# Kernel optimization log

Hardware: AMD Instinct MI355X
Metric: run time of the kernel (lower is better)

Reference implementation:

```python
import jax, jax.numpy as jnp
import numpy as np

B, S, D = 4, 4096, 1024
E, H, TOPK = 8, 2752, 2


def setup_inputs() -> dict:
    key = jax.random.key(0)
    k0, k1, k2, k3, k4 = jax.random.split(key, 5)
    x = jax.random.normal(k0, (B, S, D), dtype=jnp.float32)
    gate_w = jax.random.normal(k1, (E, D), dtype=jnp.float32) * 0.02
    w1 = jax.random.normal(k2, (E, H, D), dtype=jnp.float32) * 0.02
    w2 = jax.random.normal(k3, (E, D, H), dtype=jnp.float32) * 0.02
    w3 = jax.random.normal(k4, (E, H, D), dtype=jnp.float32) * 0.02
    return {"x": x, "gate_w": gate_w, "w1": w1, "w2": w2, "w3": w3}


def reference(x, gate_w, w1, w2, w3):
    """MoE layer: softmax router -> top-k (normalized) -> per-expert SwiGLU FFN -> weighted combine."""
    b, s, d = x.shape
    xt = x.reshape(-1, d)                       # [T, D], T = B*S
    logits = xt @ gate_w.T                      # [T, E]
    scores = jax.nn.softmax(logits, axis=-1)
    topk_w, topk_i = jax.lax.top_k(scores, TOPK)  # [T, K]
    topk_w = topk_w / (jnp.sum(topk_w, axis=-1, keepdims=True) + 1e-20)

    y = jnp.zeros_like(xt)
    n_experts = gate_w.shape[0]
    for e in range(n_experts):
        # combine weight for expert e per token (0 if not routed to e)
        we = jnp.sum(jnp.where(topk_i == e, topk_w, 0.0), axis=-1)  # [T]
        h = jax.nn.silu(xt @ w1[e].T) * (xt @ w3[e].T)              # [T, H]
        y = y + we[:, None] * (h @ w2[e].T)                         # [T, D]
    return y.reshape(b, s, d)
```

## Files before the change

kernel.cpp:

```cpp
#include <hip/hip_runtime.h>
#include <hip/hip_bf16.h>
#include <stdint.h>

#define T_TOK 16384
#define D_DIM 1024
#define E_NUM 8
#define H_DIM 2752
#define NSLOT (T_TOK * 2)

typedef __bf16 bf16x8_t __attribute__((ext_vector_type(8)));
typedef float f32x4_t __attribute__((ext_vector_type(4)));

__device__ __forceinline__ uint16_t f2bf(float f) {
    union { float f; uint32_t u; } v; v.f = f;
    return (uint16_t)((v.u + 0x7FFFu + ((v.u >> 16) & 1u)) >> 16);
}
__device__ __forceinline__ ushort4 f4_to_bf4(float4 v) {
    ushort4 r; r.x = f2bf(v.x); r.y = f2bf(v.y); r.z = f2bf(v.z); r.w = f2bf(v.w);
    return r;
}
__device__ __forceinline__ void gl_lds16(const uint16_t* g, uint16_t* l) {
    __builtin_amdgcn_global_load_lds((const __attribute__((address_space(1))) void*)g,
                                     (__attribute__((address_space(3))) void*)l,
                                     16, 0, 0);
}

__global__ __launch_bounds__(256) void router_kernel(
    const float* __restrict__ x, const float* __restrict__ gw,
    int* __restrict__ topk_i, float* __restrict__ topk_w) {
    int tid = threadIdx.x;
    int t = blockIdx.x * 4 + (tid >> 6);
    int lane = tid & 63;
    const float* xr = x + (size_t)t * D_DIM;
    double acc[E_NUM];
#pragma unroll
    for (int e = 0; e < E_NUM; ++e) acc[e] = 0.0;
    for (int k = lane; k < D_DIM; k += 64) {
        double xv = (double)xr[k];
#pragma unroll
        for (int e = 0; e < E_NUM; ++e) acc[e] += xv * (double)gw[e * D_DIM + k];
    }
#pragma unroll
    for (int e = 0; e < E_NUM; ++e) {
        double v = acc[e];
        for (int off = 32; off > 0; off >>= 1) v += __shfl_down(v, off, 64);
        acc[e] = v;
    }
    if (lane == 0) {
        int i0 = 0; double m0 = acc[0];
#pragma unroll
        for (int e = 1; e < E_NUM; ++e) if (acc[e] > m0) { m0 = acc[e]; i0 = e; }
        int i1 = -1; double m1 = -1.0e300;
#pragma unroll
        for (int e = 0; e < E_NUM; ++e) if (e != i0 && acc[e] > m1) { m1 = acc[e]; i1 = e; }
        double e1 = exp(m1 - m0);
        double s = 1.0 + e1;
        topk_i[t * 2 + 0] = i0; topk_i[t * 2 + 1] = i1;
        topk_w[t * 2 + 0] = (float)(1.0 / s);
        topk_w[t * 2 + 1] = (float)(e1 / s);
    }
}

__global__ __launch_bounds__(256) void count_kernel(
    const int* __restrict__ topk_i,
    int* __restrict__ counts_f, int* __restrict__ counts_s) {
    __shared__ int hf[E_NUM], hs[E_NUM];
    int tid = threadIdx.x;
    if (tid < E_NUM) { hf[tid] = 0; hs[tid] = 0; }
    __syncthreads();
    int t = blockIdx.x * 256 + tid;
    atomicAdd(&hf[topk_i[t * 2 + 0]], 1);
    atomicAdd(&hs[topk_i[t * 2 + 1]], 1);
    __syncthreads();
    if (tid < E_NUM) {
        if (hf[tid]) atomicAdd(&counts_f[tid], hf[tid]);
    } else if (tid < 2 * E_NUM) {
        int e = tid - E_NUM;
        if (hs[e]) atomicAdd(&counts_s[e], hs[e]);
    }
}

__global__ void prefix_kernel(const int* __restrict__ cf, const int* __restrict__ cs,
                              int* __restrict__ bases, int* __restrict__ splits,
                              int* __restrict__ cnts) {
    int s = 0;
    for (int e = 0; e < E_NUM; ++e) {
        bases[e] = s;
        splits[e] = s + cf[e];
        cnts[e] = cf[e] + cs[e];
        s += cnts[e];
    }
}

__global__ __launch_bounds__(256) void assign_kernel(
    const int* __restrict__ topk_i, const float* __restrict__ topk_w,
    const int* __restrict__ bases, const int* __restrict__ splits,
    int* __restrict__ fills_f, int* __restrict__ fills_s,
    int* __restrict__ slot_tok, float* __restrict__ slot_w) {
    __shared__ int hf[E_NUM], hs[E_NUM], bf[E_NUM], bs[E_NUM];
    int tid = threadIdx.x;
    if (tid < E_NUM) { hf[tid] = 0; hs[tid] = 0; }
    __syncthreads();
    int t = blockIdx.x * 256 + tid;
    int e0 = topk_i[t * 2 + 0], e1 = topk_i[t * 2 + 1];
    int r0 = atomicAdd(&hf[e0], 1);
    int r1 = atomicAdd(&hs[e1], 1);
    __syncthreads();
    if (tid < E_NUM) {
        bf[tid] = hf[tid] ? atomicAdd(&fills_f[tid], hf[tid]) : 0;
    } else if (tid < 2 * E_NUM) {
        int e = tid - E_NUM;
        bs[e] = hs[e] ? atomicAdd(&fills_s[e], hs[e]) : 0;
    }
    __syncthreads();
    int s0 = bases[e0] + bf[e0] + r0;
    int s1 = splits[e1] + bs[e1] + r1;
    slot_tok[s0] = t; slot_w[s0] = topk_w[t * 2 + 0];
    slot_tok[s1] = t; slot_w[s1] = topk_w[t * 2 + 1];
}

__global__ __launch_bounds__(256) void cvtx_kernel(const float* __restrict__ x,
                                                   uint16_t* __restrict__ Xb) {
    size_t i = (size_t)blockIdx.x * 256 + threadIdx.x;
    ((ushort4*)Xb)[i] = f4_to_bf4(((const float4*)x)[i]);
}
__global__ __launch_bounds__(256) void cvt13g_kernel(const float* __restrict__ w1,
                                                     const float* __restrict__ w3,
                                                     uint16_t* __restrict__ w1be,
                                                     uint16_t* __restrict__ w3be, int g) {
    size_t i = (size_t)blockIdx.x * 256 + threadIdx.x;
    size_t off = (size_t)g * 4 * H_DIM * D_DIM / 4;
    ((ushort4*)w1be)[i] = f4_to_bf4(((const float4*)w1)[off + i]);
    ((ushort4*)w3be)[i] = f4_to_bf4(((const float4*)w3)[off + i]);
}
__global__ __launch_bounds__(256) void cvt2_kernel(const float* __restrict__ w2,
                                                   uint16_t* __restrict__ w2b) {
    size_t i = (size_t)blockIdx.x * 256 + threadIdx.x;
    ((ushort4*)w2b)[i] = f4_to_bf4(((const float4*)w2)[i]);
}


__global__ __launch_bounds__(256) void gemm1_kernel(
    const uint16_t* __restrict__ Xb, const uint16_t* __restrict__ w1be,
    const uint16_t* __restrict__ w3be, const int* __restrict__ slot_tok,
    const int* __restrict__ cnts, const int* __restrict__ bases,
    uint16_t* __restrict__ hidden, int g) {
    int ez = blockIdx.z;
    int e = g * 4 + ez;
    int cnt = cnts[e];
    int m0 = blockIdx.y * 128;
    if (m0 >= cnt) return;
    int n0 = blockIdx.x * 64;
    int base = bases[e];
    const uint16_t* w1p = w1be + (size_t)ez * H_DIM * D_DIM;
    const uint16_t* w3p = w3be + (size_t)ez * H_DIM * D_DIM;

    __shared__ __align__(16) uint16_t As[3][128 * 32];
    __shared__ __align__(16) uint16_t B1s[3][64 * 32];
    __shared__ __align__(16) uint16_t B3s[3][64 * 32];

    int tid = threadIdx.x;
    int w = tid >> 6, lane = tid & 63;
    int rA = lane & 15, kq = lane >> 4;
    int lr = lane >> 2, lc = lane & 3;
    int slr = (lr >> 1) & 3;
    int ks = kq ^ ((rA >> 1) & 3);

    int tok0 = slot_tok[base + min(m0 + w * 32 + lr, cnt - 1)];
    int tok1 = slot_tok[base + min(m0 + w * 32 + 16 + lr, cnt - 1)];
    const uint16_t* pA0 = Xb + (size_t)tok0 * D_DIM + (lc ^ slr) * 8;
    const uint16_t* pA1 = Xb + (size_t)tok1 * D_DIM + (lc ^ slr) * 8;
    const uint16_t* pB1 = w1p + (size_t)(n0 + w * 16 + lr) * D_DIM + (lc ^ slr) * 8;
    const uint16_t* pB3 = w3p + (size_t)(n0 + w * 16 + lr) * D_DIM + (lc ^ slr) * 8;

    f32x4_t acc1[2][4], acc3[2][4];
#pragma unroll
    for (int r = 0; r < 2; ++r)
#pragma unroll
        for (int n = 0; n < 4; ++n) {
            acc1[r][n] = (f32x4_t){0.f, 0.f, 0.f, 0.f};
            acc3[r][n] = (f32x4_t){0.f, 0.f, 0.f, 0.f};
        }

#define G1_STAGE(bi) do {                                   \
        gl_lds16(pA0, &As[bi][(w * 2 + 0) * 512]);          \
        gl_lds16(pA1, &As[bi][(w * 2 + 1) * 512]);          \
        gl_lds16(pB1, &B1s[bi][w * 512]);                   \
        gl_lds16(pB3, &B3s[bi][w * 512]);                   \
        pA0 += 32; pA1 += 32; pB1 += 32; pB3 += 32; } while (0)

    G1_STAGE(0);
    G1_STAGE(1);
    for (int t = 0; t < 32; ++t) {
        if (t < 31) { asm volatile("s_waitcnt vmcnt(4)" ::: "memory"); }
        else        { asm volatile("s_waitcnt vmcnt(0)" ::: "memory"); }
        __builtin_amdgcn_s_barrier();
        if (t < 30) G1_STAGE((t + 2) % 3);
        int c = t % 3;

        bf16x8_t a0 = *(const bf16x8_t*)&As[c][(w * 32 + rA) * 32 + ks * 8];
        bf16x8_t a1 = *(const bf16x8_t*)&As[c][(w * 32 + 16 + rA) * 32 + ks * 8];
#pragma unroll
        for (int n = 0; n < 4; ++n) {
            bf16x8_t b1 = *(const bf16x8_t*)&B1s[c][(n * 16 + rA) * 32 + ks * 8];
            bf16x8_t b3 = *(const bf16x8_t*)&B3s[c][(n * 16 + rA) * 32 + ks * 8];
            acc1[0][n] = __builtin_amdgcn_mfma_f32_16x16x32_bf16(a0, b1, acc1[0][n], 0, 0, 0);
            acc1[1][n] = __builtin_amdgcn_mfma_f32_16x16x32_bf16(a1, b1, acc1[1][n], 0, 0, 0);
            acc3[0][n] = __builtin_amdgcn_mfma_f32_16x16x32_bf16(a0, b3, acc3[0][n], 0, 0, 0);
            acc3[1][n] = __builtin_amdgcn_mfma_f32_16x16x32_bf16(a1, b3, acc3[1][n], 0, 0, 0);
        }
    }
#undef G1_STAGE

#pragma unroll
    for (int r = 0; r < 2; ++r)
#pragma unroll
        for (int n = 0; n < 4; ++n)
#pragma unroll
            for (int i = 0; i < 4; ++i) {
                int mrow = m0 + w * 32 + r * 16 + kq * 4 + i;
                if (mrow < cnt) {
                    float gv = acc1[r][n][i];
                    float s = gv / (1.0f + __expf(-gv));
                    float h = s * acc3[r][n][i];
                    hidden[(size_t)(base + mrow) * H_DIM + n0 + n * 16 + rA] = f2bf(h);
                }
            }
}

__global__ __launch_bounds__(256) void gemm2_kernel(
    const uint16_t* __restrict__ hidden, const uint16_t* __restrict__ w2b,
    const int* __restrict__ cnts, const int* __restrict__ bases,
    const int* __restrict__ slot_tok, const float* __restrict__ slot_w,
    float* __restrict__ out) {
    int e = blockIdx.z;
    int cnt = cnts[e];
    int lin = blockIdx.y * 8 + blockIdx.x;
    int c8 = lin & 7, j = lin >> 3;
    int m_t = (j >> 3) * 8 + c8;
    int x_t = j & 7;
    int m0 = m_t * 128;
    if (m0 >= cnt) return;
    int base = bases[e];
    int d0 = x_t * 128;

    __shared__ __align__(16) uint16_t As[3][128 * 32];
    __shared__ __align__(16) uint16_t Bs[3][128 * 32];

    int tid = threadIdx.x;
    int w = tid >> 6, lane = tid & 63;
    int rA = lane & 15, kq = lane >> 4;
    int lr = lane >> 2, lc = lane & 3;
    int slr = (lr >> 1) & 3;
    int ks = kq ^ ((rA >> 1) & 3);
    int mh = w & 1, nh = w >> 1;

    int sl0 = base + min(m0 + w * 32 + lr, cnt - 1);
    int sl1 = base + min(m0 + w * 32 + 16 + lr, cnt - 1);
    const uint16_t* pA0 = hidden + (size_t)sl0 * H_DIM + (lc ^ slr) * 8;
    const uint16_t* pA1 = hidden + (size_t)sl1 * H_DIM + (lc ^ slr) * 8;
    const uint16_t* pB0 = w2b + (size_t)(e * D_DIM + d0 + w * 32 + lr) * H_DIM + (lc ^ slr) * 8;
    const uint16_t* pB1 = w2b + (size_t)(e * D_DIM + d0 + w * 32 + 16 + lr) * H_DIM + (lc ^ slr) * 8;

    f32x4_t acc[4][4];
#pragma unroll
    for (int mf = 0; mf < 4; ++mf)
#pragma unroll
        for (int nf = 0; nf < 4; ++nf) acc[mf][nf] = (f32x4_t){0.f, 0.f, 0.f, 0.f};

#define G2_STAGE(bi) do {                                   \
        gl_lds16(pA0, &As[bi][(w * 2 + 0) * 512]);          \
        gl_lds16(pA1, &As[bi][(w * 2 + 1) * 512]);          \
        gl_lds16(pB0, &Bs[bi][(w * 2 + 0) * 512]);          \
        gl_lds16(pB1, &Bs[bi][(w * 2 + 1) * 512]);          \
        pA0 += 32; pA1 += 32; pB0 += 32; pB1 += 32; } while (0)

    G2_STAGE(0);
    G2_STAGE(1);
    for (int t = 0; t < 86; ++t) {
        if (t < 85) { asm volatile("s_waitcnt vmcnt(4)" ::: "memory"); }
        else        { asm volatile("s_waitcnt vmcnt(0)" ::: "memory"); }
        __builtin_amdgcn_s_barrier();
        if (t < 84) G2_STAGE((t + 2) % 3);
        int c = t % 3;

        bf16x8_t a[4], b[4];
#pragma unroll
        for (int mf = 0; mf < 4; ++mf)
            a[mf] = *(const bf16x8_t*)&As[c][(mh * 64 + mf * 16 + rA) * 32 + ks * 8];
#pragma unroll
        for (int nf = 0; nf < 4; ++nf)
            b[nf] = *(const bf16x8_t*)&Bs[c][(nh * 64 + nf * 16 + rA) * 32 + ks * 8];
#pragma unroll
        for (int mf = 0; mf < 4; ++mf)
#pragma unroll
            for (int nf = 0; nf < 4; ++nf)
                acc[mf][nf] = __builtin_amdgcn_mfma_f32_16x16x32_bf16(a[mf], b[nf], acc[mf][nf], 0, 0, 0);
    }
#undef G2_STAGE

#pragma unroll
    for (int mf = 0; mf < 4; ++mf)
#pragma unroll
        for (int i = 0; i < 4; ++i) {
            int mr = m0 + mh * 64 + mf * 16 + kq * 4 + i;
            if (mr < cnt) {
                int slot = base + mr;
                float wgt = slot_w[slot];
                int tok = slot_tok[slot];
                float* yr = out + (size_t)tok * D_DIM + d0 + nh * 64;
#pragma unroll
                for (int nf = 0; nf < 4; ++nf)
                    atomicAdd(&yr[nf * 16 + rA], wgt * acc[mf][nf][i]);
            }
        }
}

extern "C" void kernel_launch(void* const* d_in, const int* in_sizes, int n_in,
                              void* d_out, int out_size, void* d_ws, size_t ws_size,
                              hipStream_t stream) {
    const float* x  = (const float*)d_in[0];
    const float* gw = (const float*)d_in[1];
    const float* w1 = (const float*)d_in[2];
    const float* w2 = (const float*)d_in[3];
    const float* w3 = (const float*)d_in[4];
    float* out = (float*)d_out;
    char* ws = (char*)d_ws;

    int*   counts_f = (int*)(ws + 0);
    int*   counts_s = (int*)(ws + 256);
    int*   fills_f  = (int*)(ws + 512);
    int*   fills_s  = (int*)(ws + 768);
    int*   bases    = (int*)(ws + 1024);
    int*   splits   = (int*)(ws + 1280);
    int*   cnts     = (int*)(ws + 1536);
    int*   topk_i   = (int*)(ws + 4096);
    float* topk_w   = (float*)(ws + 4096 + 1 * 131072);
    int*   slot_tok = (int*)(ws + 4096 + 2 * 131072);
    float* slot_w   = (float*)(ws + 4096 + 3 * 131072);

    const size_t HID_OFF = 4ull << 20;
    const size_t W_OFF   = HID_OFF + (size_t)NSLOT * H_DIM * 2;
    const size_t W1SZ    = (size_t)H_DIM * D_DIM * 2;
    uint16_t* hidden = (uint16_t*)(ws + HID_OFF);
    uint16_t* w1be   = (uint16_t*)(ws + W_OFF);
    uint16_t* w3be   = (uint16_t*)(ws + W_OFF + 4 * W1SZ);
    uint16_t* w2b    = (uint16_t*)(ws + W_OFF);
    uint16_t* Xb     = (uint16_t*)d_out;

    hipMemsetAsync(ws, 0, 1024, stream);

    router_kernel<<<T_TOK / 4, 256, 0, stream>>>(x, gw, topk_i, topk_w);
    count_kernel<<<T_TOK / 256, 256, 0, stream>>>(topk_i, counts_f, counts_s);
    prefix_kernel<<<1, 1, 0, stream>>>(counts_f, counts_s, bases, splits, cnts);
    assign_kernel<<<T_TOK / 256, 256, 0, stream>>>(topk_i, topk_w, bases, splits,
                                                   fills_f, fills_s, slot_tok, slot_w);
    cvtx_kernel<<<T_TOK * D_DIM / 1024, 256, 0, stream>>>(x, Xb);

    for (int g = 0; g < 2; ++g) {
        cvt13g_kernel<<<H_DIM * 4, 256, 0, stream>>>(w1, w3, w1be, w3be, g);
        gemm1_kernel<<<dim3(H_DIM / 64, 128, 4), 256, 0, stream>>>(
            Xb, w1be, w3be, slot_tok, cnts, bases, hidden, g);
    }

    hipMemsetAsync(out, 0, (size_t)T_TOK * D_DIM * sizeof(float), stream);
    cvt2_kernel<<<E_NUM * D_DIM * H_DIM / 1024, 256, 0, stream>>>(w2, w2b);
    gemm2_kernel<<<dim3(8, 128, E_NUM), 256, 0, stream>>>(
        hidden, w2b, cnts, bases, slot_tok, slot_w, out);
}
```

Baseline: 1.274 ms.

## Enlarge MoE GEMM tiles to 256-row, 8-wave blocks with interleaved load/MFMA phases

Both expert GEMMs move from 256-thread blocks with 128x64 or 128x128 tiles to 512-thread blocks with 256x128 (gemm1) and 256x256 (gemm2) tiles. Each K-step is split into four phases that alternate LDS fragment reads, global-to-LDS prefetch issue and MFMA bursts, using barriers, sched_barrier and s_setprio. The aim is more data reuse per byte loaded and better overlap of memory traffic with matrix math. In exchange the kernels use more LDS and registers per block, add more barriers, and launch fewer blocks; the H dimension now needs bounds guards because 2752 is not a multiple of 128.

After: 1.291 ms. Within noise of the previous version (+1.4%).

```diff
diff --git a/kernel.cpp b/kernel.cpp
--- a/kernel.cpp
+++ b/kernel.cpp
@@ -24,6 +24,8 @@
                                      (__attribute__((address_space(3))) void*)l,
                                      16, 0, 0);
 }
+
+#define MFMA16(a, b, c) __builtin_amdgcn_mfma_f32_16x16x32_bf16(a, b, c, 0, 0, 0)
 
 __global__ __launch_bounds__(256) void router_kernel(
     const float* __restrict__ x, const float* __restrict__ gw,
@@ -140,7 +142,7 @@
 }
 
 
-__global__ __launch_bounds__(256) void gemm1_kernel(
+__global__ __launch_bounds__(512, 2) void gemm1_kernel(
     const uint16_t* __restrict__ Xb, const uint16_t* __restrict__ w1be,
     const uint16_t* __restrict__ w3be, const int* __restrict__ slot_tok,
     const int* __restrict__ cnts, const int* __restrict__ bases,
@@ -148,167 +150,285 @@
     int ez = blockIdx.z;
     int e = g * 4 + ez;
     int cnt = cnts[e];
-    int m0 = blockIdx.y * 128;
+    int m0 = blockIdx.y * 256;
     if (m0 >= cnt) return;
-    int n0 = blockIdx.x * 64;
+    int n0 = blockIdx.x * 128;
     int base = bases[e];
     const uint16_t* w1p = w1be + (size_t)ez * H_DIM * D_DIM;
     const uint16_t* w3p = w3be + (size_t)ez * H_DIM * D_DIM;
 
-    __shared__ __align__(16) uint16_t As[3][128 * 32];
-    __shared__ __align__(16) uint16_t B1s[3][64 * 32];
-    __shared__ __align__(16) uint16_t B3s[3][64 * 32];
+    __shared__ __align__(16) uint16_t As[3][256 * 32];
+    __shared__ __align__(16) uint16_t B1s[3][128 * 32];
+    __shared__ __align__(16) uint16_t B3s[3][128 * 32];
 
     int tid = threadIdx.x;
     int w = tid >> 6, lane = tid & 63;
+    int wr = w >> 2, wc = w & 3;
     int rA = lane & 15, kq = lane >> 4;
-    int lr = lane >> 2, lc = lane & 3;
-    int slr = (lr >> 1) & 3;
     int ks = kq ^ ((rA >> 1) & 3);
-
-    int tok0 = slot_tok[base + min(m0 + w * 32 + lr, cnt - 1)];
-    int tok1 = slot_tok[base + min(m0 + w * 32 + 16 + lr, cnt - 1)];
-    const uint16_t* pA0 = Xb + (size_t)tok0 * D_DIM + (lc ^ slr) * 8;
-    const uint16_t* pA1 = Xb + (size_t)tok1 * D_DIM + (lc ^ slr) * 8;
-    const uint16_t* pB1 = w1p + (size_t)(n0 + w * 16 + lr) * D_DIM + (lc ^ slr) * 8;
-    const uint16_t* pB3 = w3p + (size_t)(n0 + w * 16 + lr) * D_DIM + (lc ^ slr) * 8;
-
-    f32x4_t acc1[2][4], acc3[2][4];
-#pragma unroll
-    for (int r = 0; r < 2; ++r)
-#pragma unroll
-        for (int n = 0; n < 4; ++n) {
-            acc1[r][n] = (f32x4_t){0.f, 0.f, 0.f, 0.f};
-            acc3[r][n] = (f32x4_t){0.f, 0.f, 0.f, 0.f};
-        }
-
-#define G1_STAGE(bi) do {                                   \
-        gl_lds16(pA0, &As[bi][(w * 2 + 0) * 512]);          \
-        gl_lds16(pA1, &As[bi][(w * 2 + 1) * 512]);          \
-        gl_lds16(pB1, &B1s[bi][w * 512]);                   \
-        gl_lds16(pB3, &B3s[bi][w * 512]);                   \
-        pA0 += 32; pA1 += 32; pB1 += 32; pB3 += 32; } while (0)
-
-    G1_STAGE(0);
-    G1_STAGE(1);
+    int r = tid >> 2, c = tid & 3;
+    int cs = c ^ ((r >> 1) & 3);
+
+    int slA0 = base + min(m0 + r, cnt - 1);
+    int slA1 = base + min(m0 + 128 + r, cnt - 1);
+    const uint16_t* pA0 = Xb + (size_t)slot_tok[slA0] * D_DIM + cs * 8;
+    const uint16_t* pA1 = Xb + (size_t)slot_tok[slA1] * D_DIM + cs * 8;
+    int nB = min(n0 + r, H_DIM - 1);
+    const uint16_t* pB1 = w1p + (size_t)nB * D_DIM + cs * 8;
+    const uint16_t* pB3 = w3p + (size_t)nB * D_DIM + cs * 8;
+
+    f32x4_t acc1[8][2], acc3[8][2];
+#pragma unroll
+    for (int mf = 0; mf < 8; ++mf)
+#pragma unroll
+        for (int nf = 0; nf < 2; ++nf) {
+            acc1[mf][nf] = (f32x4_t){0.f, 0.f, 0.f, 0.f};
+            acc3[mf][nf] = (f32x4_t){0.f, 0.f, 0.f, 0.f};
+        }
+
+#define G1_STA0(s) gl_lds16(pA0, &As[s][w * 512])
+#define G1_STA1(s) gl_lds16(pA1, &As[s][4096 + w * 512])
+#define G1_STB1(s) gl_lds16(pB1, &B1s[s][w * 512])
+#define G1_STB3(s) gl_lds16(pB3, &B3s[s][w * 512])
+#define G1_ADV() do { pA0 += 32; pA1 += 32; pB1 += 32; pB3 += 32; } while (0)
+
+    G1_STA0(0); G1_STA1(0); G1_STB1(0); G1_STB3(0); G1_ADV();
+    G1_STA0(1); G1_STA1(1); G1_STB1(1); G1_STB3(1); G1_ADV();
+    asm volatile("s_waitcnt vmcnt(4)" ::: "memory");
+    __builtin_amdgcn_s_barrier();
+
     for (int t = 0; t < 32; ++t) {
-        if (t < 31) { asm volatile("s_waitcnt vmcnt(4)" ::: "memory"); }
-        else        { asm volatile("s_waitcnt vmcnt(0)" ::: "memory"); }
-        __builtin_amdgcn_s_barrier();
-        if (t < 30) G1_STAGE((t + 2) % 3);
-        int c = t % 3;
-
-        bf16x8_t a0 = *(const bf16x8_t*)&As[c][(w * 32 + rA) * 32 + ks * 8];
-        bf16x8_t a1 = *(const bf16x8_t*)&As[c][(w * 32 + 16 + rA) * 32 + ks * 8];
-#pragma unroll
-        for (int n = 0; n < 4; ++n) {
-            bf16x8_t b1 = *(const bf16x8_t*)&B1s[c][(n * 16 + rA) * 32 + ks * 8];
-            bf16x8_t b3 = *(const bf16x8_t*)&B3s[c][(n * 16 + rA) * 32 + ks * 8];
-            acc1[0][n] = __builtin_amdgcn_mfma_f32_16x16x32_bf16(a0, b1, acc1[0][n], 0, 0, 0);
-            acc1[1][n] = __builtin_amdgcn_mfma_f32_16x16x32_bf16(a1, b1, acc1[1][n], 0, 0, 0);
-            acc3[0][n] = __builtin_amdgcn_mfma_f32_16x16x32_bf16(a0, b3, acc3[0][n], 0, 0, 0);
-            acc3[1][n] = __builtin_amdgcn_mfma_f32_16x16x32_bf16(a1, b3, acc3[1][n], 0, 0, 0);
-        }
-    }
-#undef G1_STAGE
-
-#pragma unroll
-    for (int r = 0; r < 2; ++r)
-#pragma unroll
-        for (int n = 0; n < 4; ++n)
-#pragma unroll
-            for (int i = 0; i < 4; ++i) {
-                int mrow = m0 + w * 32 + r * 16 + kq * 4 + i;
-                if (mrow < cnt) {
-                    float gv = acc1[r][n][i];
-                    float s = gv / (1.0f + __expf(-gv));
-                    float h = s * acc3[r][n][i];
-                    hidden[(size_t)(base + mrow) * H_DIM + n0 + n * 16 + rA] = f2bf(h);
+        int cur = t % 3, nst = (t + 2) % 3;
+        bool st = (t + 2 < 32);
+        const uint16_t* A = As[cur];
+        const uint16_t* B1 = B1s[cur];
+        const uint16_t* B3 = B3s[cur];
+        bf16x8_t a[4], b1[2], b3[2];
+
+#pragma unroll
+        for (int mf = 0; mf < 4; ++mf)
+            a[mf] = *(const bf16x8_t*)&A[(wr * 128 + mf * 16 + rA) * 32 + ks * 8];
+        b1[0] = *(const bf16x8_t*)&B1[(wc * 32 + rA) * 32 + ks * 8];
+        b1[1] = *(const bf16x8_t*)&B1[(wc * 32 + 16 + rA) * 32 + ks * 8];
+        if (st) G1_STA0(nst);
+        __builtin_amdgcn_s_barrier();
+        asm volatile("s_waitcnt lgkmcnt(0)" ::: "memory");
+        __builtin_amdgcn_sched_barrier(0);
+        __builtin_amdgcn_s_setprio(1);
+#pragma unroll
+        for (int mf = 0; mf < 4; ++mf) {
+            acc1[mf][0] = MFMA16(a[mf], b1[0], acc1[mf][0]);
+            acc1[mf][1] = MFMA16(a[mf], b1[1], acc1[mf][1]);
+        }
+        __builtin_amdgcn_s_setprio(0);
+        __builtin_amdgcn_s_barrier();
+
+        b3[0] = *(const bf16x8_t*)&B3[(wc * 32 + rA) * 32 + ks * 8];
+        b3[1] = *(const bf16x8_t*)&B3[(wc * 32 + 16 + rA) * 32 + ks * 8];
+        if (st) G1_STA1(nst);
+        __builtin_amdgcn_s_barrier();
+        asm volatile("s_waitcnt lgkmcnt(0)" ::: "memory");
+        __builtin_amdgcn_sched_barrier(0);
+        __builtin_amdgcn_s_setprio(1);
+#pragma unroll
+        for (int mf = 0; mf < 4; ++mf) {
+            acc3[mf][0] = MFMA16(a[mf], b3[0], acc3[mf][0]);
+            acc3[mf][1] = MFMA16(a[mf], b3[1], acc3[mf][1]);
+        }
+        __builtin_amdgcn_s_setprio(0);
+        __builtin_amdgcn_s_barrier();
+
+#pragma unroll
+        for (int mf = 0; mf < 4; ++mf)
+            a[mf] = *(const bf16x8_t*)&A[(wr * 128 + (mf + 4) * 16 + rA) * 32 + ks * 8];
+        if (st) G1_STB1(nst);
+        __builtin_amdgcn_s_barrier();
+        asm volatile("s_waitcnt lgkmcnt(0)" ::: "memory");
+        __builtin_amdgcn_sched_barrier(0);
+        __builtin_amdgcn_s_setprio(1);
+#pragma unroll
+        for (int mf = 0; mf < 4; ++mf) {
+            acc1[mf + 4][0] = MFMA16(a[mf], b1[0], acc1[mf + 4][0]);
+            acc1[mf + 4][1] = MFMA16(a[mf], b1[1], acc1[mf + 4][1]);
+        }
+        __builtin_amdgcn_s_setprio(0);
+        __builtin_amdgcn_s_barrier();
+
+        if (st) { G1_STB3(nst); G1_ADV(); }
+        __builtin_amdgcn_s_barrier();
+        __builtin_amdgcn_s_setprio(1);
+#pragma unroll
+        for (int mf = 0; mf < 4; ++mf) {
+            acc3[mf + 4][0] = MFMA16(a[mf], b3[0], acc3[mf + 4][0]);
+            acc3[mf + 4][1] = MFMA16(a[mf], b3[1], acc3[mf + 4][1]);
+        }
+        __builtin_amdgcn_s_setprio(0);
+        if (t < 31) {
+            if (t == 30) asm volatile("s_waitcnt vmcnt(0)" ::: "memory");
+            else         asm volatile("s_waitcnt vmcnt(4)" ::: "memory");
+            __builtin_amdgcn_s_barrier();
+        }
+    }
+#undef G1_STA0
+#undef G1_STA1
+#undef G1_STB1
+#undef G1_STB3
+#undef G1_ADV
+
+#pragma unroll
+    for (int mf = 0; mf < 8; ++mf)
+#pragma unroll
+        for (int i = 0; i < 4; ++i) {
+            int mrow = m0 + wr * 128 + mf * 16 + kq * 4 + i;
+            if (mrow < cnt) {
+#pragma unroll
+                for (int nf = 0; nf < 2; ++nf) {
+                    int col = n0 + wc * 32 + nf * 16 + rA;
+                    if (col < H_DIM) {
+                        float gv = acc1[mf][nf][i];
+                        float s = gv / (1.0f + __expf(-gv));
+                        float h = s * acc3[mf][nf][i];
+                        hidden[(size_t)(base + mrow) * H_DIM + col] = f2bf(h);
+                    }
                 }
             }
-}
-
-__global__ __launch_bounds__(256) void gemm2_kernel(
+        }
+}
+
+__global__ __launch_bounds__(512, 2) void gemm2_kernel(
     const uint16_t* __restrict__ hidden, const uint16_t* __restrict__ w2b,
     const int* __restrict__ cnts, const int* __restrict__ bases,
     const int* __restrict__ slot_tok, const float* __restrict__ slot_w,
     float* __restrict__ out) {
     int e = blockIdx.z;
     int cnt = cnts[e];
-    int lin = blockIdx.y * 8 + blockIdx.x;
-    int c8 = lin & 7, j = lin >> 3;
-    int m_t = (j >> 3) * 8 + c8;
-    int x_t = j & 7;
-    int m0 = m_t * 128;
+    int m0 = blockIdx.y * 256;
     if (m0 >= cnt) return;
     int base = bases[e];
-    int d0 = x_t * 128;
-
-    __shared__ __align__(16) uint16_t As[3][128 * 32];
-    __shared__ __align__(16) uint16_t Bs[3][128 * 32];
+    int d0 = blockIdx.x * 256;
+
+    __shared__ __align__(16) uint16_t As[3][256 * 32];
+    __shared__ __align__(16) uint16_t Bs[3][256 * 32];
 
     int tid = threadIdx.x;
     int w = tid >> 6, lane = tid & 63;
+    int wr = w >> 2, wc = w & 3;
     int rA = lane & 15, kq = lane >> 4;
-    int lr = lane >> 2, lc = lane & 3;
-    int slr = (lr >> 1) & 3;
     int ks = kq ^ ((rA >> 1) & 3);
-    int mh = w & 1, nh = w >> 1;
-
-    int sl0 = base + min(m0 + w * 32 + lr, cnt - 1);
-    int sl1 = base + min(m0 + w * 32 + 16 + lr, cnt - 1);
-    const uint16_t* pA0 = hidden + (size_t)sl0 * H_DIM + (lc ^ slr) * 8;
-    const uint16_t* pA1 = hidden + (size_t)sl1 * H_DIM + (lc ^ slr) * 8;
-    const uint16_t* pB0 = w2b + (size_t)(e * D_DIM + d0 + w * 32 + lr) * H_DIM + (lc ^ slr) * 8;
-    const uint16_t* pB1 = w2b + (size_t)(e * D_DIM + d0 + w * 32 + 16 + lr) * H_DIM + (lc ^ slr) * 8;
-
-    f32x4_t acc[4][4];
-#pragma unroll
-    for (int mf = 0; mf < 4; ++mf)
+    int r = tid >> 2, c = tid & 3;
+    int cs = c ^ ((r >> 1) & 3);
+
+    int slA0 = base + min(m0 + r, cnt - 1);
+    int slA1 = base + min(m0 + 128 + r, cnt - 1);
+    const uint16_t* pA0 = hidden + (size_t)slA0 * H_DIM + cs * 8;
+    const uint16_t* pA1 = hidden + (size_t)slA1 * H_DIM + cs * 8;
+    const uint16_t* pB0 = w2b + (size_t)(e * D_DIM + d0 + r) * H_DIM + cs * 8;
+    const uint16_t* pB1 = w2b + (size_t)(e * D_DIM + d0 + 128 + r) * H_DIM + cs * 8;
+
+    f32x4_t acc[8][4];
+#pragma unroll
+    for (int mf = 0; mf < 8; ++mf)
 #pragma unroll
         for (int nf = 0; nf < 4; ++nf) acc[mf][nf] = (f32x4_t){0.f, 0.f, 0.f, 0.f};
 
-#define G2_STAGE(bi) do {                                   \
-        gl_lds16(pA0, &As[bi][(w * 2 + 0) * 512]);          \
-        gl_lds16(pA1, &As[bi][(w * 2 + 1) * 512]);          \
-        gl_lds16(pB0, &Bs[bi][(w * 2 + 0) * 512]);          \
-        gl_lds16(pB1, &Bs[bi][(w * 2 + 1) * 512]);          \
-        pA0 += 32; pA1 += 32; pB0 += 32; pB1 += 32; } while (0)
-
-    G2_STAGE(0);
-    G2_STAGE(1);
+#define G2_STA0(s) gl_lds16(pA0, &As[s][w * 512])
+#define G2_STA1(s) gl_lds16(pA1, &As[s][4096 + w * 512])
+#define G2_STB0(s) gl_lds16(pB0, &Bs[s][w * 512])
+#define G2_STB1(s) gl_lds16(pB1, &Bs[s][4096 + w * 512])
+#define G2_ADV() do { pA0 += 32; pA1 += 32; pB0 += 32; pB1 += 32; } while (0)
+
+    G2_STA0(0); G2_STA1(0); G2_STB0(0); G2_STB1(0); G2_ADV();
+    G2_STA0(1); G2_STA1(1); G2_STB0(1); G2_STB1(1); G2_ADV();
+    asm volatile("s_waitcnt vmcnt(4)" ::: "memory");
+    __builtin_amdgcn_s_barrier();
+
     for (int t = 0; t < 86; ++t) {
-        if (t < 85) { asm volatile("s_waitcnt vmcnt(4)" ::: "memory"); }
-        else        { asm volatile("s_waitcnt vmcnt(0)" ::: "memory"); }
-        __builtin_amdgcn_s_barrier();
-        if (t < 84) G2_STAGE((t + 2) % 3);
-        int c = t % 3;
-
+        int cur = t % 3, nst = (t + 2) % 3;
+        bool st = (t + 2 < 86);
+        const uint16_t* A = As[cur];
+        const uint16_t* B = Bs[cur];
         bf16x8_t a[4], b[4];
+
 #pragma unroll
         for (int mf = 0; mf < 4; ++mf)
-            a[mf] = *(const bf16x8_t*)&As[c][(mh * 64 + mf * 16 + rA) * 32 + ks * 8];
-#pragma unroll
-        for (int nf = 0; nf < 4; ++nf)
-            b[nf] = *(const bf16x8_t*)&Bs[c][(nh * 64 + nf * 16 + rA) * 32 + ks * 8];
+            a[mf] = *(const bf16x8_t*)&A[(wr * 128 + mf * 16 + rA) * 32 + ks * 8];
+        b[0] = *(const bf16x8_t*)&B[(wc * 64 + rA) * 32 + ks * 8];
+        b[1] = *(const bf16x8_t*)&B[(wc * 64 + 16 + rA) * 32 + ks * 8];
+        if (st) G2_STA0(nst);
+        __builtin_amdgcn_s_barrier();
+        asm volatile("s_waitcnt lgkmcnt(0)" ::: "memory");
+        __builtin_amdgcn_sched_barrier(0);
+        __builtin_amdgcn_s_setprio(1);
+#pragma unroll
+        for (int mf = 0; mf < 4; ++mf) {
+            acc[mf][0] = MFMA16(a[mf], b[0], acc[mf][0]);
+            acc[mf][1] = MFMA16(a[mf], b[1], acc[mf][1]);
+        }
+        __builtin_amdgcn_s_setprio(0);
+        __builtin_amdgcn_s_barrier();
+
+        b[2] = *(const bf16x8_t*)&B[(wc * 64 + 32 + rA) * 32 + ks * 8];
+        b[3] = *(const bf16x8_t*)&B[(wc * 64 + 48 + rA) * 32 + ks * 8];
+        if (st) G2_STA1(nst);
+        __builtin_amdgcn_s_barrier();
+        asm volatile("s_waitcnt lgkmcnt(0)" ::: "memory");
+        __builtin_amdgcn_sched_barrier(0);
+        __builtin_amdgcn_s_setprio(1);
+#pragma unroll
+        for (int mf = 0; mf < 4; ++mf) {
+            acc[mf][2] = MFMA16(a[mf], b[2], acc[mf][2]);
+            acc[mf][3] = MFMA16(a[mf], b[3], acc[mf][3]);
+        }
+        __builtin_amdgcn_s_setprio(0);
+        __builtin_amdgcn_s_barrier();
+
 #pragma unroll
         for (int mf = 0; mf < 4; ++mf)
-#pragma unroll
-            for (int nf = 0; nf < 4; ++nf)
-                acc[mf][nf] = __builtin_amdgcn_mfma_f32_16x16x32_bf16(a[mf], b[nf], acc[mf][nf], 0, 0, 0);
-    }
-#undef G2_STAGE
-
-#pragma unroll
-    for (int mf = 0; mf < 4; ++mf)
+            a[mf] = *(const bf16x8_t*)&A[(wr * 128 + (mf + 4) * 16 + rA) * 32 + ks * 8];
+        if (st) G2_STB0(nst);
+        __builtin_amdgcn_s_barrier();
+        asm volatile("s_waitcnt lgkmcnt(0)" ::: "memory");
+        __builtin_amdgcn_sched_barrier(0);
+        __builtin_amdgcn_s_setprio(1);
+#pragma unroll
+        for (int mf = 0; mf < 4; ++mf) {
+            acc[mf + 4][0] = MFMA16(a[mf], b[0], acc[mf + 4][0]);
+            acc[mf + 4][1] = MFMA16(a[mf], b[1], acc[mf + 4][1]);
+        }
+        __builtin_amdgcn_s_setprio(0);
+        __builtin_amdgcn_s_barrier();
+
+        if (st) { G2_STB1(nst); G2_ADV(); }
+        __builtin_amdgcn_s_barrier();
+        __builtin_amdgcn_s_setprio(1);
+#pragma unroll
+        for (int mf = 0; mf < 4; ++mf) {
+            acc[mf + 4][2] = MFMA16(a[mf], b[2], acc[mf + 4][2]);
+            acc[mf + 4][3] = MFMA16(a[mf], b[3], acc[mf + 4][3]);
+        }
+        __builtin_amdgcn_s_setprio(0);
+        if (t < 85) {
+            if (t == 84) asm volatile("s_waitcnt vmcnt(0)" ::: "memory");
+            else         asm volatile("s_waitcnt vmcnt(4)" ::: "memory");
+            __builtin_amdgcn_s_barrier();
+        }
+    }
+#undef G2_STA0
+#undef G2_STA1
+#undef G2_STB0
+#undef G2_STB1
+#undef G2_ADV
+
+#pragma unroll
+    for (int mf = 0; mf < 8; ++mf)
 #pragma unroll
         for (int i = 0; i < 4; ++i) {
-            int mr = m0 + mh * 64 + mf * 16 + kq * 4 + i;
+            int mr = m0 + wr * 128 + mf * 16 + kq * 4 + i;
             if (mr < cnt) {
                 int slot = base + mr;
                 float wgt = slot_w[slot];
                 int tok = slot_tok[slot];
-                float* yr = out + (size_t)tok * D_DIM + d0 + nh * 64;
+                float* yr = out + (size_t)tok * D_DIM + d0 + wc * 64;
 #pragma unroll
                 for (int nf = 0; nf < 4; ++nf)
                     atomicAdd(&yr[nf * 16 + rA], wgt * acc[mf][nf][i]);
@@ -359,12 +479,12 @@
 
     for (int g = 0; g < 2; ++g) {
         cvt13g_kernel<<<H_DIM * 4, 256, 0, stream>>>(w1, w3, w1be, w3be, g);
-        gemm1_kernel<<<dim3(H_DIM / 64, 128, 4), 256, 0, stream>>>(
+        gemm1_kernel<<<dim3(22, 128, 4), 512, 0, stream>>>(
             Xb, w1be, w3be, slot_tok, cnts, bases, hidden, g);
     }
 
     hipMemsetAsync(out, 0, (size_t)T_TOK * D_DIM * sizeof(float), stream);
     cvt2_kernel<<<E_NUM * D_DIM * H_DIM / 1024, 256, 0, stream>>>(w2, w2b);
-    gemm2_kernel<<<dim3(8, 128, E_NUM), 256, 0, stream>>>(
+    gemm2_kernel<<<dim3(4, 128, 8), 512, 0, stream>>>(
         hidden, w2b, cnts, bases, slot_tok, slot_w, out);
 }
```
